# Kernel optimization log

Hardware: AMD Instinct MI355X
Metric: run time of the kernel (lower is better)

The kernel has to match this reference:

```python
import jax, jax.numpy as jnp
import numpy as np

NB_TF = 4          # brightness, contrast, invert-blend, gain
MAGS_PER_TF = 9    # magnitudes 0.1 .. 0.9 (range(1, int(mag*10)) with mag=1)
NB_OP = NB_TF * MAGS_PER_TF


def setup_inputs() -> dict:
    key = jax.random.key(0)
    k1, k2, k3 = jax.random.split(key, 3)
    B, C, H, W = 256, 3, 224, 224
    x = jax.random.uniform(k1, (B, C, H, W), dtype=jnp.float32)
    # per-image sampled op index (Categorical over a uniform distribution)
    sample = jax.random.randint(k2, (B,), 0, NB_OP)
    # per-op Bernoulli(prob=0.5) coin: 1 -> apply the op, 0 -> identity
    apply_mask = jax.random.randint(k3, (NB_OP,), 0, 2).astype(jnp.int32)
    return {"x": x, "sample": sample, "apply_mask": apply_mask}


def _apply_ops(x, sample, apply_mask):
    # Decode op index -> (tf type, magnitude). op_list layout: for tf in TFs:
    #   for m in 1..9: (tf, prob, m/10)
    tf_idx = sample // MAGS_PER_TF                       # [B]
    mag = ((sample % MAGS_PER_TF) + 1).astype(x.dtype) / 10.0
    mag = mag[:, None, None, None]                       # [B,1,1,1]

    mean = jnp.mean(x, axis=(1, 2, 3), keepdims=True)    # per-image mean
    t_bright = jnp.clip(x + mag, 0.0, 1.0)               # brightness shift
    t_contr = jnp.clip(mean + (x - mean) * (1.0 + mag), 0.0, 1.0)
    t_inv = (1.0 - mag) * x + mag * (1.0 - x)            # blend with inverted
    t_gain = jnp.clip(x * (1.0 + mag), 0.0, 1.0)         # multiplicative gain

    stack = jnp.stack([t_bright, t_contr, t_inv, t_gain], axis=1)  # [B,4,C,H,W]
    sel = tf_idx[:, None, None, None, None]              # [B,1,1,1,1]
    transformed = jnp.take_along_axis(stack, sel, axis=1)[:, 0]    # [B,C,H,W]

    applied = (apply_mask[sample] > 0)[:, None, None, None]
    return jnp.where(applied, transformed, x)


def reference(x, sample, apply_mask):
    # N_seqTF = 1 -> single round of sample -> gather -> transform -> scatter,
    # here expressed as a fully vectorized per-image select.
    return _apply_ops(x, sample, apply_mask)
```

## Files before the change

kernel.cpp:

```cpp
#include <hip/hip_runtime.h>

#define N_IMG   256
#define HW      (224 * 224)
#define CHW     (3 * HW)
#define V4      (CHW / 4)
#define THREADS 256

#define PARTS       7
#define PART_V4     (V4 / PARTS)
#define PER_THREAD  (PART_V4 / THREADS)

#define CHUNKS  (V4 / THREADS)
#define U       7
#define ABLK    (CHUNKS / U)

#define MAGS_PER_TF 9

typedef float f4 __attribute__((ext_vector_type(4)));

__device__ __forceinline__ float clip01(float v) {
    return fminf(fmaxf(v, 0.0f), 1.0f);
}

__global__ __launch_bounds__(THREADS) void mean_kernel(
        const float* __restrict__ x,
        const int* __restrict__ sample,
        const int* __restrict__ apply_mask,
        float* __restrict__ partials ) {
    const int img  = blockIdx.y;
    const int part = blockIdx.x;
    const int s    = sample[img];
    const int tf   = s / MAGS_PER_TF;
    if (tf != 1 || apply_mask[s] <= 0) return;

    const f4* xp = (const f4*)x + (size_t)img * V4 + (size_t)part * PART_V4;
    float sum = 0.0f;
#pragma unroll
    for (int k = 0; k < PER_THREAD; ++k) {
        f4 v = xp[threadIdx.x + k * THREADS];
        sum += (v.x + v.y) + (v.z + v.w);
    }
#pragma unroll
    for (int off = 32; off > 0; off >>= 1)
        sum += __shfl_down(sum, off, 64);

    __shared__ float wsum[THREADS / 64];
    if ((threadIdx.x & 63) == 0) wsum[threadIdx.x >> 6] = sum;
    __syncthreads();
    if (threadIdx.x == 0) {
        float t = (wsum[0] + wsum[1]) + (wsum[2] + wsum[3]);
        partials[img * PARTS + part] = t;
    }
}

__global__ __launch_bounds__(THREADS) void apply_kernel(
        const float* __restrict__ x,
        const int* __restrict__ sample,
        const int* __restrict__ apply_mask,
        const float* __restrict__ partials,
        float* __restrict__ out) {
    const int img = blockIdx.y;
    const int b   = blockIdx.x;
    const int s   = sample[img];
    const int tf  = s / MAGS_PER_TF;
    const float mag = (float)(s % MAGS_PER_TF + 1) / 10.0f;
    const bool applied = apply_mask[s] > 0;

    float mean = 0.0f;
    if (applied && tf == 1) {
        float m = 0.0f;
#pragma unroll
        for (int p = 0; p < PARTS; ++p) m += partials[img * PARTS + p];
        mean = m / (float)CHW;
    }

    const size_t base = (size_t)img * V4 + (size_t)b * (U * THREADS) + threadIdx.x;
    const f4* xp = (const f4*)x;
    f4*       op = (f4*)out;

    f4 v[U];
#pragma unroll
    for (int k = 0; k < U; ++k) v[k] = xp[base + (size_t)k * THREADS];

    f4 r[U];
    if (!applied) {
#pragma unroll
        for (int k = 0; k < U; ++k) r[k] = v[k];
    } else if (tf == 0) {
#pragma unroll
        for (int k = 0; k < U; ++k) {
            r[k].x = clip01(v[k].x + mag);
            r[k].y = clip01(v[k].y + mag);
            r[k].z = clip01(v[k].z + mag);
            r[k].w = clip01(v[k].w + mag);
        }
    } else if (tf == 1) {
        const float g = 1.0f + mag;
#pragma unroll
        for (int k = 0; k < U; ++k) {
            r[k].x = clip01(mean + (v[k].x - mean) * g);
            r[k].y = clip01(mean + (v[k].y - mean) * g);
            r[k].z = clip01(mean + (v[k].z - mean) * g);
            r[k].w = clip01(mean + (v[k].w - mean) * g);
        }
    } else if (tf == 2) {
        const float a = 1.0f - mag;
#pragma unroll
        for (int k = 0; k < U; ++k) {
            r[k].x = a * v[k].x + mag * (1.0f - v[k].x);
            r[k].y = a * v[k].y + mag * (1.0f - v[k].y);
            r[k].z = a * v[k].z + mag * (1.0f - v[k].z);
            r[k].w = a * v[k].w + mag * (1.0f - v[k].w);
        }
    } else {
        const float g = 1.0f + mag;
#pragma unroll
        for (int k = 0; k < U; ++k) {
            r[k].x = clip01(v[k].x * g);
            r[k].y = clip01(v[k].y * g);
            r[k].z = clip01(v[k].z * g);
            r[k].w = clip01(v[k].w * g);
        }
    }

#pragma unroll
    for (int k = 0; k < U; ++k)
        __builtin_nontemporal_store(r[k], op + base + (size_t)k * THREADS);
}

extern "C" void kernel_launch(void* const* d_in, const int* in_sizes, int n_in,
                              void* d_out, int out_size, void* d_ws, size_t ws_size,
                              hipStream_t stream) {
    const float* x          = (const float*)d_in[0];
    const int*   sample     = (const int*)d_in[1];
    const int*   apply_mask = (const int*)d_in[2];
    float*       out        = (float*)d_out;
    float*       partials   = (float*)d_ws;

    dim3 mgrid(PARTS, N_IMG);
    mean_kernel<<<mgrid, THREADS, 0, stream>>>(x, sample, apply_mask, partials);

    dim3 agrid(ABLK, N_IMG);
    apply_kernel<<<agrid, THREADS, 0, stream>>>(x, sample, apply_mask, partials, out);
}
```

Baseline: 275.5 us.

## Fuse mean reduction into apply kernel with per-image atomic grid barrier

Merges the separate mean-reduction kernel into the apply kernel. Each block sums its own tile, adds it atomically to a per-image total, then spin-waits until all blocks of that image have arrived before applying the contrast transform. This avoids reading contrast images twice and saves a kernel launch, but it adds a memset and relies on all blocks of an image being resident at the same time, which risks deadlock. It also switches nontemporal stores to plain stores.

```diff
diff --git a/kernel.cpp b/kernel.cpp
--- a/kernel.cpp
+++ b/kernel.cpp
@@ -5,10 +5,6 @@
 #define CHW     (3 * HW)
 #define V4      (CHW / 4)
 #define THREADS 256
-
-#define PARTS       7
-#define PART_V4     (V4 / PARTS)
-#define PER_THREAD  (PART_V4 / THREADS)
 
 #define CHUNKS  (V4 / THREADS)
 #define U       7
@@ -22,42 +18,12 @@
     return fminf(fmaxf(v, 0.0f), 1.0f);
 }
 
-__global__ __launch_bounds__(THREADS) void mean_kernel(
+__global__ __launch_bounds__(THREADS) void fused_kernel(
         const float* __restrict__ x,
         const int* __restrict__ sample,
         const int* __restrict__ apply_mask,
-        float* __restrict__ partials ) {
-    const int img  = blockIdx.y;
-    const int part = blockIdx.x;
-    const int s    = sample[img];
-    const int tf   = s / MAGS_PER_TF;
-    if (tf != 1 || apply_mask[s] <= 0) return;
-
-    const f4* xp = (const f4*)x + (size_t)img * V4 + (size_t)part * PART_V4;
-    float sum = 0.0f;
-#pragma unroll
-    for (int k = 0; k < PER_THREAD; ++k) {
-        f4 v = xp[threadIdx.x + k * THREADS];
-        sum += (v.x + v.y) + (v.z + v.w);
-    }
-#pragma unroll
-    for (int off = 32; off > 0; off >>= 1)
-        sum += __shfl_down(sum, off, 64);
-
-    __shared__ float wsum[THREADS / 64];
-    if ((threadIdx.x & 63) == 0) wsum[threadIdx.x >> 6] = sum;
-    __syncthreads();
-    if (threadIdx.x == 0) {
-        float t = (wsum[0] + wsum[1]) + (wsum[2] + wsum[3]);
-        partials[img * PARTS + part] = t;
-    }
-}
-
-__global__ __launch_bounds__(THREADS) void apply_kernel(
-        const float* __restrict__ x,
-        const int* __restrict__ sample,
-        const int* __restrict__ apply_mask,
-        const float* __restrict__ partials,
+        float* __restrict__ gsum ,
+        int*   __restrict__ gcnt ,
         float* __restrict__ out) {
     const int img = blockIdx.y;
     const int b   = blockIdx.x;
@@ -65,14 +31,6 @@
     const int tf  = s / MAGS_PER_TF;
     const float mag = (float)(s % MAGS_PER_TF + 1) / 10.0f;
     const bool applied = apply_mask[s] > 0;
-
-    float mean = 0.0f;
-    if (applied && tf == 1) {
-        float m = 0.0f;
-#pragma unroll
-        for (int p = 0; p < PARTS; ++p) m += partials[img * PARTS + p];
-        mean = m / (float)CHW;
-    }
 
     const size_t base = (size_t)img * V4 + (size_t)b * (U * THREADS) + threadIdx.x;
     const f4* xp = (const f4*)x;
@@ -82,50 +40,78 @@
 #pragma unroll
     for (int k = 0; k < U; ++k) v[k] = xp[base + (size_t)k * THREADS];
 
-    f4 r[U];
-    if (!applied) {
+    float mean = 0.0f;
+    if (applied && tf == 1) {
+        float ps = 0.0f;
 #pragma unroll
-        for (int k = 0; k < U; ++k) r[k] = v[k];
-    } else if (tf == 0) {
+        for (int k = 0; k < U; ++k)
+            ps += (v[k].x + v[k].y) + (v[k].z + v[k].w);
 #pragma unroll
-        for (int k = 0; k < U; ++k) {
-            r[k].x = clip01(v[k].x + mag);
-            r[k].y = clip01(v[k].y + mag);
-            r[k].z = clip01(v[k].z + mag);
-            r[k].w = clip01(v[k].w + mag);
+        for (int off = 32; off > 0; off >>= 1)
+            ps += __shfl_down(ps, off, 64);
+
+        __shared__ float wsum[THREADS / 64];
+        __shared__ float smean;
+        if ((threadIdx.x & 63) == 0) wsum[threadIdx.x >> 6] = ps;
+        __syncthreads();
+        if (threadIdx.x == 0) {
+            float t = (wsum[0] + wsum[1]) + (wsum[2] + wsum[3]);
+            atomicAdd(&gsum[img], t);
+            __threadfence();
+            atomicAdd(&gcnt[img], 1);
+            while (__hip_atomic_load(&gcnt[img], __ATOMIC_ACQUIRE,
+                                     __HIP_MEMORY_SCOPE_AGENT) < ABLK)
+                __builtin_amdgcn_s_sleep(2);
+            float tot = __hip_atomic_load(&gsum[img], __ATOMIC_RELAXED,
+                                          __HIP_MEMORY_SCOPE_AGENT);
+            smean = tot / (float)CHW;
         }
-    } else if (tf == 1) {
-        const float g = 1.0f + mag;
+        __syncthreads();
+        mean = smean;
+    }
+
+    if (applied) {
+        if (tf == 0) {
 #pragma unroll
-        for (int k = 0; k < U; ++k) {
-            r[k].x = clip01(mean + (v[k].x - mean) * g);
-            r[k].y = clip01(mean + (v[k].y - mean) * g);
-            r[k].z = clip01(mean + (v[k].z - mean) * g);
-            r[k].w = clip01(mean + (v[k].w - mean) * g);
-        }
-    } else if (tf == 2) {
-        const float a = 1.0f - mag;
+            for (int k = 0; k < U; ++k) {
+                v[k].x = clip01(v[k].x + mag);
+                v[k].y = clip01(v[k].y + mag);
+                v[k].z = clip01(v[k].z + mag);
+                v[k].w = clip01(v[k].w + mag);
+            }
+        } else if (tf == 1) {
+            const float g = 1.0f + mag;
 #pragma unroll
-        for (int k = 0; k < U; ++k) {
-            r[k].x = a * v[k].x + mag * (1.0f - v[k].x);
-            r[k].y = a * v[k].y + mag * (1.0f - v[k].y);
-            r[k].z = a * v[k].z + mag * (1.0f - v[k].z);
-            r[k].w = a * v[k].w + mag * (1.0f - v[k].w);
-        }
-    } else {
-        const float g = 1.0f + mag;
+            for (int k = 0; k < U; ++k) {
+                v[k].x = clip01(mean + (v[k].x - mean) * g);
+                v[k].y = clip01(mean + (v[k].y - mean) * g);
+                v[k].z = clip01(mean + (v[k].z - mean) * g);
+                v[k].w = clip01(mean + (v[k].w - mean) * g);
+            }
+        } else if (tf == 2) {
+            const float a = 1.0f - mag;
 #pragma unroll
-        for (int k = 0; k < U; ++k) {
-            r[k].x = clip01(v[k].x * g);
-            r[k].y = clip01(v[k].y * g);
-            r[k].z = clip01(v[k].z * g);
-            r[k].w = clip01(v[k].w * g);
+            for (int k = 0; k < U; ++k) {
+                v[k].x = a * v[k].x + mag * (1.0f - v[k].x);
+                v[k].y = a * v[k].y + mag * (1.0f - v[k].y);
+                v[k].z = a * v[k].z + mag * (1.0f - v[k].z);
+                v[k].w = a * v[k].w + mag * (1.0f - v[k].w);
+            }
+        } else {
+            const float g = 1.0f + mag;
+#pragma unroll
+            for (int k = 0; k < U; ++k) {
+                v[k].x = clip01(v[k].x * g);
+                v[k].y = clip01(v[k].y * g);
+                v[k].z = clip01(v[k].z * g);
+                v[k].w = clip01(v[k].w * g);
+            }
         }
     }
 
 #pragma unroll
     for (int k = 0; k < U; ++k)
-        __builtin_nontemporal_store(r[k], op + base + (size_t)k * THREADS);
+        op[base + (size_t)k * THREADS] = v[k];
 }
 
 extern "C" void kernel_launch(void* const* d_in, const int* in_sizes, int n_in,
@@ -135,11 +121,12 @@
     const int*   sample     = (const int*)d_in[1];
     const int*   apply_mask = (const int*)d_in[2];
     float*       out        = (float*)d_out;
-    float*       partials   = (float*)d_ws;
+    float*       gsum       = (float*)d_ws;
+    int*         gcnt       = (int*)d_ws + N_IMG;
 
-    dim3 mgrid(PARTS, N_IMG);
-    mean_kernel<<<mgrid, THREADS, 0, stream>>>(x, sample, apply_mask, partials);
+    hipMemsetAsync(d_ws, 0, 2 * N_IMG * sizeof(float), stream);
 
-    dim3 agrid(ABLK, N_IMG);
-    apply_kernel<<<agrid, THREADS, 0, stream>>>(x, sample, apply_mask, partials, out);
+    dim3 grid(ABLK, N_IMG);
+    fused_kernel<<<grid, THREADS, 0, stream>>>(x, sample, apply_mask,
+                                               gsum, gcnt, out);
 }
```

New measurement: 307.8 us. 11.7% more time.
